# Optimization experiments

Measured on AMD Instinct MI355X. Metric: run time of the kernel, lower is better.

Reference implementation:

```python
import jax, jax.numpy as jnp
import numpy as np
from jax import lax

V_TH = 1.0    # init kwarg 'thresh'
ALPHA = 1.0   # init kwarg 'alpha' (surrogate-gradient width, unused in fwd)

T, B, N = 32, 32, 65536


def setup_inputs() -> dict:
    key = jax.random.key(0)
    x = jax.random.normal(key, (T, B, N), dtype=jnp.float32)
    return {"x": x}


def reference(x) -> jnp.ndarray:
    # Integrate-and-fire neuron, TBN layout, sequential scan over time:
    #   m_t = v_{t-1} + x_t            (integrate)
    #   y_t = heaviside(m_t - v_th)    (fire)
    #   v_t = m_t - y_t * v_th         (soft reset by subtraction)
    def step(v, x_t):
        m = v + x_t
        y = (m >= V_TH).astype(x_t.dtype)
        v_new = m - y * V_TH
        return v_new, y

    v0 = jnp.zeros_like(x[0])
    _, y_seq = lax.scan(step, v0, x)
    return y_seq
```

## Files before the change

### kernel.cpp

```cpp
#include <hip/hip_runtime.h>


typedef float v4f __attribute__((ext_vector_type(4)));

#define T_STEPS 32

__global__ __launch_bounds__(256, 8) void if_kernel(const v4f* __restrict__ x,
                                                    v4f* __restrict__ y,
                                                    int bn4) {
    int idx = blockIdx.x * blockDim.x + threadIdx.x;
    if (idx >= bn4) return;

    const v4f* xp = x + idx;

    float v0 = 0.f, v1 = 0.f, v2 = 0.f, v3 = 0.f;
    unsigned m0 = 0u, m1 = 0u, m2 = 0u, m3 = 0u;

#pragma unroll
    for (int t = 0; t < T_STEPS; ++t) {
        v4f xv = xp[(size_t)t * bn4];
        float a0 = v0 + xv.x;
        float a1 = v1 + xv.y;
        float a2 = v2 + xv.z;
        float a3 = v3 + xv.w;
        bool s0 = a0 >= 1.0f;
        bool s1 = a1 >= 1.0f;
        bool s2 = a2 >= 1.0f;
        bool s3 = a3 >= 1.0f;
        m0 |= (unsigned)s0 << t;
        m1 |= (unsigned)s1 << t;
        m2 |= (unsigned)s2 << t;
        m3 |= (unsigned)s3 << t;
        v0 = s0 ? a0 - 1.0f : a0;
        v1 = s1 ? a1 - 1.0f : a1;
        v2 = s2 ? a2 - 1.0f : a2;
        v3 = s3 ? a3 - 1.0f : a3;
    }

    v4f* yp = y + idx;
#pragma unroll
    for (int t = 0; t < T_STEPS; ++t) {
        v4f out;
        out.x = ((m0 >> t) & 1u) ? 1.0f : 0.0f;
        out.y = ((m1 >> t) & 1u) ? 1.0f : 0.0f;
        out.z = ((m2 >> t) & 1u) ? 1.0f : 0.0f;
        out.w = ((m3 >> t) & 1u) ? 1.0f : 0.0f;
        __builtin_nontemporal_store(out, yp + (size_t)t * bn4);
    }
}

extern "C" void kernel_launch(void* const* d_in, const int* in_sizes, int n_in,
                              void* d_out, int out_size, void* d_ws, size_t ws_size,
                              hipStream_t stream) {
    const float* x = (const float*)d_in[0];
    float* y = (float*)d_out;

    int total = in_sizes[0];
    int bn = total / T_STEPS;
    int bn4 = bn / 4;

    int block = 256;
    int grid = (bn4 + block - 1) / block;

    if_kernel<<<grid, block, 0, stream>>>((const v4f*)x, (v4f*)y, bn4);
}
```

Measured before the change: 458.1 us.

## Issue input loads via inline asm with staged waitcnt pipelining

Replaces the compiler-scheduled loop of loads with inline-assembly global_load_dwordx4 batches. It issues 24 loads up front and then 8 more mid-scan, with explicit s_waitcnt vmcnt thresholds so the compute on early timesteps overlaps the outstanding loads. It also drops the occupancy hint from launch_bounds, so the compiler may use more VGPRs for the 32 in-flight vectors. The aim is deeper memory-level parallelism per thread on this bandwidth-bound kernel, at the cost of lower occupancy and fragile hand-written asm (correctness depends on waitcnt ordering and the compiler not reordering around volatile asm).

```diff
diff --git a/kernel.cpp b/kernel.cpp
--- a/kernel.cpp
+++ b/kernel.cpp
@@ -5,39 +5,87 @@
 
 #define T_STEPS 32
 
-__global__ __launch_bounds__(256, 8) void if_kernel(const v4f* __restrict__ x,
-                                                    v4f* __restrict__ y,
-                                                    int bn4) {
+#define IF_STEP(xv, t)                                \
+    do {                                              \
+        float a0 = v0 + (xv).x;                       \
+        float a1 = v1 + (xv).y;                       \
+        float a2 = v2 + (xv).z;                       \
+        float a3 = v3 + (xv).w;                       \
+        bool s0 = a0 >= 1.0f;                         \
+        bool s1 = a1 >= 1.0f;                         \
+        bool s2 = a2 >= 1.0f;                         \
+        bool s3 = a3 >= 1.0f;                         \
+        m0 |= (unsigned)s0 << (t);                    \
+        m1 |= (unsigned)s1 << (t);                    \
+        m2 |= (unsigned)s2 << (t);                    \
+        m3 |= (unsigned)s3 << (t);                    \
+        v0 = s0 ? a0 - 1.0f : a0;                     \
+        v1 = s1 ? a1 - 1.0f : a1;                     \
+        v2 = s2 ? a2 - 1.0f : a2;                     \
+        v3 = s3 ? a3 - 1.0f : a3;                     \
+    } while (0)
+
+#define LD(i) "global_load_dwordx4 %" #i ", %24, %26\n\t" \
+              "v_add_u32 %24, %25, %24\n\t"
+
+#define LD2(i) "global_load_dwordx4 %" #i ", %16, %18\n\t" \
+               "v_add_u32 %16, %17, %16\n\t"
+
+__global__ __launch_bounds__(256) void if_kernel(const float* __restrict__ x,
+                                                 float* __restrict__ y,
+                                                 int bn4) {
     int idx = blockIdx.x * blockDim.x + threadIdx.x;
     if (idx >= bn4) return;
 
-    const v4f* xp = x + idx;
+    unsigned voff = (unsigned)idx * 16u;
+    unsigned stride = (unsigned)bn4 * 16u;
+
+    v4f d0, d1, d2, d3, d4, d5, d6, d7, d8, d9, d10, d11,
+        d12, d13, d14, d15, d16, d17, d18, d19, d20, d21, d22, d23;
+    v4f e0, e1, e2, e3, e4, e5, e6, e7;
+
+    asm volatile(
+        LD(0) LD(1) LD(2) LD(3) LD(4) LD(5) LD(6) LD(7)
+        LD(8) LD(9) LD(10) LD(11) LD(12) LD(13) LD(14) LD(15)
+        LD(16) LD(17) LD(18) LD(19) LD(20) LD(21) LD(22) LD(23)
+        "s_waitcnt vmcnt(8)\n\t"
+        : "=v"(d0), "=v"(d1), "=v"(d2), "=v"(d3), "=v"(d4), "=v"(d5),
+          "=v"(d6), "=v"(d7), "=v"(d8), "=v"(d9), "=v"(d10), "=v"(d11),
+          "=v"(d12), "=v"(d13), "=v"(d14), "=v"(d15), "=v"(d16), "=v"(d17),
+          "=v"(d18), "=v"(d19), "=v"(d20), "=v"(d21), "=v"(d22), "=v"(d23),
+          "+v"(voff)
+        : "s"(stride), "s"(x));
 
     float v0 = 0.f, v1 = 0.f, v2 = 0.f, v3 = 0.f;
     unsigned m0 = 0u, m1 = 0u, m2 = 0u, m3 = 0u;
 
-#pragma unroll
-    for (int t = 0; t < T_STEPS; ++t) {
-        v4f xv = xp[(size_t)t * bn4];
-        float a0 = v0 + xv.x;
-        float a1 = v1 + xv.y;
-        float a2 = v2 + xv.z;
-        float a3 = v3 + xv.w;
-        bool s0 = a0 >= 1.0f;
-        bool s1 = a1 >= 1.0f;
-        bool s2 = a2 >= 1.0f;
-        bool s3 = a3 >= 1.0f;
-        m0 |= (unsigned)s0 << t;
-        m1 |= (unsigned)s1 << t;
-        m2 |= (unsigned)s2 << t;
-        m3 |= (unsigned)s3 << t;
-        v0 = s0 ? a0 - 1.0f : a0;
-        v1 = s1 ? a1 - 1.0f : a1;
-        v2 = s2 ? a2 - 1.0f : a2;
-        v3 = s3 ? a3 - 1.0f : a3;
-    }
+    IF_STEP(d0, 0);  IF_STEP(d1, 1);  IF_STEP(d2, 2);  IF_STEP(d3, 3);
+    IF_STEP(d4, 4);  IF_STEP(d5, 5);  IF_STEP(d6, 6);  IF_STEP(d7, 7);
+    IF_STEP(d8, 8);  IF_STEP(d9, 9);  IF_STEP(d10, 10); IF_STEP(d11, 11);
+    IF_STEP(d12, 12); IF_STEP(d13, 13); IF_STEP(d14, 14); IF_STEP(d15, 15);
 
-    v4f* yp = y + idx;
+    asm volatile(
+        LD2(0) LD2(1) LD2(2) LD2(3) LD2(4) LD2(5) LD2(6) LD2(7)
+        "s_waitcnt vmcnt(8)\n\t"
+        : "=v"(e0), "=v"(e1), "=v"(e2), "=v"(e3),
+          "=v"(e4), "=v"(e5), "=v"(e6), "=v"(e7),
+          "+v"(d16), "+v"(d17), "+v"(d18), "+v"(d19),
+          "+v"(d20), "+v"(d21), "+v"(d22), "+v"(d23),
+          "+v"(voff)
+        : "s"(stride), "s"(x));
+
+    IF_STEP(d16, 16); IF_STEP(d17, 17); IF_STEP(d18, 18); IF_STEP(d19, 19);
+    IF_STEP(d20, 20); IF_STEP(d21, 21); IF_STEP(d22, 22); IF_STEP(d23, 23);
+
+    asm volatile(
+        "s_waitcnt vmcnt(0)\n\t"
+        : "+v"(e0), "+v"(e1), "+v"(e2), "+v"(e3),
+          "+v"(e4), "+v"(e5), "+v"(e6), "+v"(e7));
+
+    IF_STEP(e0, 24); IF_STEP(e1, 25); IF_STEP(e2, 26); IF_STEP(e3, 27);
+    IF_STEP(e4, 28); IF_STEP(e5, 29); IF_STEP(e6, 30); IF_STEP(e7, 31);
+
+    v4f* yp = (v4f*)y + idx;
 #pragma unroll
     for (int t = 0; t < T_STEPS; ++t) {
         v4f out;
@@ -62,5 +110,5 @@
     int block = 256;
     int grid = (bn4 + block - 1) / block;
 
-    if_kernel<<<grid, block, 0, stream>>>((const v4f*)x, (v4f*)y, bn4);
+    if_kernel<<<grid, block, 0, stream>>>(x, y, bn4);
 }
```

New measurement: 461.4 us. No clear change (+0.7%).
